# Optimization experiments

Measured on AMD Instinct MI355X. Metric: run time of the kernel, lower is better.

## Reference

```python
import jax, jax.numpy as jnp
import numpy as np

# ---- quantization constants (8-bit, per-tensor affine; representative values) ----
Q_MAX = 255.0
S_IN, Z_IN = 0.05, 128.0      # block input
S1, Z1 = 0.04, 128.0          # after expand 1x1 + hardswish
S2, Z2 = 0.04, 128.0          # after depthwise 5x5 + hardswish
S_SE1, Z_SE1 = 0.03, 128.0    # SE fc1 output
S_SE2, Z_SE2 = 1.0 / 255.0, 0.0  # SE fc2 hardsigmoid output in [0,1]
S_MUL, Z_MUL = 0.04, 128.0    # SE gated activation
S3, Z3 = 0.05, 128.0          # after project 1x1
S_OUT, Z_OUT = 0.06, 128.0    # after residual add
W_SCALE = 0.01                # symmetric per-tensor weight scale (zero_point = 0)
EXP_C = 576                   # expanded channels (depthwise groups)


def conv(x, w, stride=1, padding=0, groups=1):
    return jax.lax.conv_general_dilated(
        x, w, (stride, stride), [(padding, padding), (padding, padding)],
        feature_group_count=groups, dimension_numbers=('NCHW', 'OIHW', 'NCHW'))


def hardswish(x):
    return x * jnp.clip(x + 3.0, 0.0, 6.0) * (1.0 / 6.0)


def hardsigmoid(x):
    return jnp.clip(x + 3.0, 0.0, 6.0) * (1.0 / 6.0)


def qconv(x_q, w_q, b_q, s_in, z_in, s_out, z_out, stride=1, padding=0, groups=1, act=None):
    """Quantized conv: int-domain accumulation (simulated in fp32), fused activation
    on the dequantized accumulator, then requantize to [0, Q_MAX]."""
    acc = conv(x_q - z_in, w_q, stride, padding, groups) + b_q[None, :, None, None]
    deq = acc * (s_in * W_SCALE)  # dequantize accumulator
    if act == 'hardswish':
        deq = hardswish(deq)
    elif act == 'hardsigmoid':
        deq = hardsigmoid(deq)
    return jnp.clip(deq * (1.0 / s_out) + z_out, 0.0, Q_MAX)


def setup_inputs() -> dict:
    key = jax.random.key(0)
    ks = jax.random.split(key, 11)
    def qw(k, shape):  # int8-style symmetric weights stored as fp32 integers
        return jnp.round(jnp.clip(jax.random.normal(k, shape) * 40.0, -127.0, 127.0))
    def qb(k, n):      # int32-style bias in accumulator domain
        return jnp.round(jax.random.normal(k, (n,)) * 500.0)
    return {
        'x':      jnp.round(jax.random.uniform(ks[0], (64, 96, 28, 28)) * Q_MAX),
        'w_exp':  qw(ks[1], (576, 96, 1, 1)),  'b_exp':  qb(ks[2], 576),
        'w_dw':   qw(ks[3], (576, 1, 5, 5)),   'b_dw':   qb(ks[4], 576),
        'w_se1':  qw(ks[5], (144, 576, 1, 1)), 'b_se1':  qb(ks[6], 144),
        'w_se2':  qw(ks[7], (576, 144, 1, 1)), 'b_se2':  qb(ks[8], 576),
        'w_proj': qw(ks[9], (96, 576, 1, 1)),  'b_proj': qb(ks[10], 96),
    }


def reference(x, w_exp, b_exp, w_dw, b_dw, w_se1, b_se1, w_se2, b_se2, w_proj, b_proj):
    # expand 1x1 (+ hardswish)
    e = qconv(x, w_exp, b_exp, S_IN, Z_IN, S1, Z1, act='hardswish')
    # depthwise 5x5, padding=(5-1)//2=2, groups=expanded (+ hardswish)
    d = qconv(e, w_dw, b_dw, S1, Z1, S2, Z2, padding=2, groups=EXP_C, act='hardswish')
    # squeeze-excitation: global avg pool -> fc1 -> fc2(hardsigmoid) -> quantized mul
    pooled = jnp.mean(d, axis=(2, 3), keepdims=True)  # [N, 576, 1, 1]
    g1 = qconv(pooled, w_se1, b_se1, S2, Z2, S_SE1, Z_SE1)
    g2 = qconv(g1, w_se2, b_se2, S_SE1, Z_SE1, S_SE2, Z_SE2, act='hardsigmoid')
    gated = jnp.clip((g2 - Z_SE2) * (d - Z2) * (S_SE2 * S2 / S_MUL) + Z_MUL, 0.0, Q_MAX)
    # project 1x1 (linear)
    p = qconv(gated, w_proj, b_proj, S_MUL, Z_MUL, S3, Z3)
    # quantized residual add (stride=1, in==out channels -> use_res_connect)
    out = jnp.clip((x - Z_IN) * (S_IN / S_OUT) + (p - Z3) * (S3 / S_OUT) + Z_OUT, 0.0, Q_MAX)
    return out
```

## Files before the change

### kernel.cpp

```cpp
#include <hip/hip_runtime.h>

typedef _Float16 v8h __attribute__((ext_vector_type(8)));
typedef _Float16 v4h __attribute__((ext_vector_type(4)));
typedef _Float16 v4h_a4 __attribute__((ext_vector_type(4), aligned(4)));
typedef _Float16 v2h __attribute__((ext_vector_type(2)));
typedef float v4f __attribute__((ext_vector_type(4)));

#define NB 64
#define CI 96
#define CE 576
#define CO 96
#define HW 784
#define SEC 144

#if defined(__has_builtin)
#if __has_builtin(__builtin_amdgcn_fdot2)
#define HAVE_FDOT2 1
#endif
#endif

__device__ __forceinline__ float fdot2(v2h a, v2h b, float c) {
#ifdef HAVE_FDOT2
  return __builtin_amdgcn_fdot2(a, b, c, false);
#else
  return (float)a[0] * (float)b[0] + ((float)a[1] * (float)b[1] + c);
#endif
}

__global__ __launch_bounds__(256) void k0_cvt_w(const float* __restrict__ w_exp,
                                                const float* __restrict__ w_proj,
                                                _Float16* __restrict__ w_exp_h,
                                                _Float16* __restrict__ w_proj_h) {
  int i = blockIdx.x * 256 + threadIdx.x;
  if (i < CE * CI) {
    w_exp_h[i]  = (_Float16)w_exp[i];
    w_proj_h[i] = (_Float16)w_proj[i];
  }
}

__global__ __launch_bounds__(384) void k1_expand(const float* __restrict__ x,
                                                 const _Float16* __restrict__ w_exp_h,
                                                 const float* __restrict__ b_exp,
                                                 _Float16* __restrict__ e_s) {
  __shared__ _Float16 xf[3 * 7 * 520];
  const int tid = threadIdx.x;
  const int n   = blockIdx.z;
  const int co0 = blockIdx.y * 96;
  const int hw0 = blockIdx.x * 112;

#pragma unroll
  for (int it = 0; it < 7; ++it) {
    int idx = it * 384 + tid;
    int c = idx / 28, seg = idx % 28;
    const float4 v = *(const float4*)&x[(n * CI + c) * HW + hw0 + seg * 4];
    int s = c >> 5, q = (c >> 3) & 3, j = c & 7;
    int t = seg >> 2, l0 = (seg & 3) * 4;
    int base = (s * 7 + t) * 520 + (q * 16 + l0) * 8 + j;
    xf[base]      = (_Float16)(v.x - 128.0f);
    xf[base + 8]  = (_Float16)(v.y - 128.0f);
    xf[base + 16] = (_Float16)(v.z - 128.0f);
    xf[base + 24] = (_Float16)(v.w - 128.0f);
  }
  __syncthreads();

  const int wv = tid >> 6, lane = tid & 63;
  const int l15 = lane & 15, q = lane >> 4;

  const _Float16* wrow = &w_exp_h[(co0 + wv * 16 + l15) * CI + q * 8];
  v8h a0 = *(const v8h*)(wrow);
  v8h a1 = *(const v8h*)(wrow + 32);
  v8h a2 = *(const v8h*)(wrow + 64);

  v4f acc[7];
#pragma unroll
  for (int t = 0; t < 7; ++t) acc[t] = (v4f){0.f, 0.f, 0.f, 0.f};

#pragma unroll
  for (int t = 0; t < 7; ++t) {
    v8h b0 = *(const v8h*)&xf[(0 * 7 + t) * 520 + lane * 8];
    v8h b1 = *(const v8h*)&xf[(1 * 7 + t) * 520 + lane * 8];
    v8h b2 = *(const v8h*)&xf[(2 * 7 + t) * 520 + lane * 8];
    acc[t] = __builtin_amdgcn_mfma_f32_16x16x32_f16(a0, b0, acc[t], 0, 0, 0);
    acc[t] = __builtin_amdgcn_mfma_f32_16x16x32_f16(a1, b1, acc[t], 0, 0, 0);
    acc[t] = __builtin_amdgcn_mfma_f32_16x16x32_f16(a2, b2, acc[t], 0, 0, 0);
  }

  float bia[4];
#pragma unroll
  for (int r = 0; r < 4; ++r) bia[r] = b_exp[co0 + wv * 16 + q * 4 + r];

#pragma unroll
  for (int t = 0; t < 7; ++t) {
#pragma unroll
    for (int r = 0; r < 4; ++r) {
      int co = co0 + wv * 16 + q * 4 + r;
      int hw = hw0 + t * 16 + l15;
      float deq = (acc[t][r] + bia[r]) * 5.0e-4f;
      float cl  = fminf(fmaxf(deq + 3.0f, 0.0f), 6.0f);
      float hs  = deq * cl * (1.0f / 6.0f);
      float ev  = fminf(fmaxf(hs * 25.0f, -128.0f), 127.0f);
      e_s[(n * CE + co) * HW + hw] = (_Float16)ev;
    }
  }
}

__global__ __launch_bounds__(256, 5) void k2_dw(const _Float16* __restrict__ e_s,
                                                const float* __restrict__ w_dw,
                                                const float* __restrict__ b_dw,
                                                _Float16* __restrict__ d_t,
                                                float* __restrict__ d_sums) {
  __shared__ _Float16 e_lds[8][32][36];
  __shared__ _Float16 w_pairs[8][5][8];
  __shared__ _Float16 d_tile[8][784];
  const int tid = threadIdx.x;
  const int n = blockIdx.y;
  const int c0 = blockIdx.x * 8;

  {
    unsigned long long* z = (unsigned long long*)&e_lds[0][0][0];
    for (int idx = tid; idx < 8 * 32 * 36 * 2 / 8; idx += 256) z[idx] = 0ull;
  }
  for (int idx = tid; idx < 320; idx += 256) {
    int c = idx / 40, r = idx % 40, dy = r / 8, k = r % 8;
    int tap = (k < 4) ? k : (k - 3);
    w_pairs[c][dy][k] = (_Float16)w_dw[(c0 + c) * 25 + dy * 5 + tap];
  }
  __syncthreads();
  for (int idx = tid; idx < 1568; idx += 256) {
    int c = idx / 196, r = idx % 196, y = r / 7, j = r % 7;
    v4h v = *(const v4h*)&e_s[(n * CE + c0 + c) * HW + y * 28 + j * 4];
    *(v4h_a4*)&e_lds[c][2 + y][6 + j * 4] = v;
  }
  __syncthreads();

  const int c = tid >> 5, l = tid & 31;
  v2h W01[5], W23[5], W12[5], W34[5];
  float W0s[5], W4s[5];
#pragma unroll
  for (int dy = 0; dy < 5; ++dy) {
    W01[dy] = *(const v2h*)&w_pairs[c][dy][0];
    W23[dy] = *(const v2h*)&w_pairs[c][dy][2];
    W12[dy] = *(const v2h*)&w_pairs[c][dy][4];
    W34[dy] = *(const v2h*)&w_pairs[c][dy][6];
    W0s[dy] = (float)W01[dy][0];
    W4s[dy] = (float)W34[dy][1];
  }
  const float bc = b_dw[c0 + c];

  float csum = 0.0f;
  if (l < 28) {
    const int y = l;
    v2h P0[5], P1[5], P2[5], P3[5];
#pragma unroll
    for (int dy = 0; dy < 5; ++dy) {
      const _Float16* row = &e_lds[c][y + dy][0];
      v4h w01 = *(const v4h*)(row + 4);
      v4h w23 = *(const v4h*)(row + 8);
      P0[dy] = (v2h){w01[0], w01[1]};
      P1[dy] = (v2h){w01[2], w01[3]};
      P2[dy] = (v2h){w23[0], w23[1]};
      P3[dy] = (v2h){w23[2], w23[3]};
    }
#pragma unroll
    for (int x0 = 0; x0 < 28; x0 += 4) {
      float o0 = bc, o1 = bc, o2 = bc, o3 = bc;
#pragma unroll
      for (int dy = 0; dy < 5; ++dy) {
        o0 = fdot2(P0[dy], W01[dy], o0);
        o0 = fdot2(P1[dy], W23[dy], o0);
        o0 += (float)P2[dy][0] * W4s[dy];
        o1 += (float)P0[dy][1] * W0s[dy];
        o1 = fdot2(P1[dy], W12[dy], o1);
        o1 = fdot2(P2[dy], W34[dy], o1);
        o2 = fdot2(P1[dy], W01[dy], o2);
        o2 = fdot2(P2[dy], W23[dy], o2);
        o2 += (float)P3[dy][0] * W4s[dy];
        o3 += (float)P1[dy][1] * W0s[dy];
        o3 = fdot2(P2[dy], W12[dy], o3);
        o3 = fdot2(P3[dy], W34[dy], o3);
      }
      v4h dv;
      float oo[4] = {o0, o1, o2, o3};
#pragma unroll
      for (int i = 0; i < 4; ++i) {
        float deq = oo[i] * 4.0e-4f;
        float cl  = fminf(fmaxf(deq + 3.0f, 0.0f), 6.0f);
        float dvv = fminf(fmaxf(deq * cl * (25.0f / 6.0f), -128.0f), 127.0f);
        dv[i] = (_Float16)dvv;
        csum += dvv;
      }
      *(v4h*)&d_tile[c][y * 28 + x0] = dv;
      if (x0 < 24) {
#pragma unroll
        for (int dy = 0; dy < 5; ++dy) {
          const _Float16* row = &e_lds[c][y + dy][0];
          v4h nw = *(const v4h*)(row + x0 + 12);
          P0[dy] = P2[dy];
          P1[dy] = P3[dy];
          P2[dy] = (v2h){nw[0], nw[1]};
          P3[dy] = (v2h){nw[2], nw[3]};
        }
      }
    }
  }
#pragma unroll
  for (int m = 16; m >= 1; m >>= 1) csum += __shfl_xor(csum, m);
  if (l == 0) d_sums[n * CE + c0 + c] = csum;

  __syncthreads();
  const size_t obase = ((size_t)n * 72 + (c0 >> 3)) * 784;
  for (int hw = tid; hw < 784; hw += 256) {
    v8h o;
#pragma unroll
    for (int j = 0; j < 8; ++j) o[j] = d_tile[j][hw];
    *(v8h*)&d_t[(obase + hw) * 8] = o;
  }
}

__global__ __launch_bounds__(256) void k3a_fc1(const float* __restrict__ d_sums,
                                               const float* __restrict__ w_se1,
                                               const float* __restrict__ b_se1,
                                               float* __restrict__ g1) {
  const int tid = threadIdx.x;
  const int wv = tid >> 6, lane = tid & 63;
  const int n = blockIdx.y;
  const int o = blockIdx.x * 4 + wv;
  const float* wrow = &w_se1[o * CE];
  const float* srow = &d_sums[n * CE];
  float p = 0.f;
#pragma unroll
  for (int s = 0; s < 9; ++s) {
    int cc = lane + s * 64;
    p += wrow[cc] * srow[cc];
  }
#pragma unroll
  for (int m = 32; m >= 1; m >>= 1) p += __shfl_xor(p, m);
  if (lane == 0) {
    float deq = (p * (1.0f / 784.0f) + b_se1[o]) * 4.0e-4f;
    g1[n * SEC + o] = fminf(fmaxf(deq * 33.3333333f + 128.0f, 0.0f), 255.0f) - 128.0f;
  }
}

__global__ __launch_bounds__(256) void k3b_fc2(const float* __restrict__ g1,
                                               const float* __restrict__ w_se2,
                                               const float* __restrict__ b_se2,
                                               _Float16* __restrict__ g2h) {
  const int tid = threadIdx.x;
  const int wv = tid >> 6, lane = tid & 63;
  const int n = blockIdx.y;
  const int o = blockIdx.x * 4 + wv;
  const float* wrow = &w_se2[o * SEC];
  const float* grow = &g1[n * SEC];
  float p = wrow[lane] * grow[lane] + wrow[lane + 64] * grow[lane + 64];
  if (lane < 16) p += wrow[lane + 128] * grow[lane + 128];
#pragma unroll
  for (int m = 32; m >= 1; m >>= 1) p += __shfl_xor(p, m);
  if (lane == 0) {
    float deq = (p + b_se2[o]) * 3.0e-4f;
    g2h[n * CE + o] =
        (_Float16)(fminf(fmaxf(deq + 3.0f, 0.0f), 6.0f) * (1.0f / 6.0f));
  }
}

__global__ __launch_bounds__(192) void k4_proj(const _Float16* __restrict__ d_t,
                                               const _Float16* __restrict__ g2h,
                                               const _Float16* __restrict__ w_proj_h,
                                               const float* __restrict__ b_proj,
                                               const float* __restrict__ x,
                                               float* __restrict__ out) {
  const int tid = threadIdx.x;
  const int n = blockIdx.z;
  const int co0 = blockIdx.y * 48;
  const int hw0 = blockIdx.x * 112;
  const int wv = tid >> 6, lane = tid & 63;
  const int l15 = lane & 15, q = lane >> 4;

  v4f acc[7];
#pragma unroll
  for (int t = 0; t < 7; ++t) acc[t] = (v4f){0.f, 0.f, 0.f, 0.f};

  const _Float16* dbase = d_t + (((size_t)n * 72 + q) * 784 + hw0 + l15) * 8;
  const _Float16* abase = &w_proj_h[(co0 + wv * 16 + l15) * CE + q * 8];
  const _Float16* gbase = &g2h[(size_t)n * CE + q * 8];

  for (int ks = 0; ks < 18; ++ks) {
    v8h a = *(const v8h*)(abase + ks * 32);
    v8h g = *(const v8h*)(gbase + ks * 32);
    v8h ag = a * g;
    const _Float16* dk = dbase + (size_t)ks * (4 * 784 * 8);
#pragma unroll
    for (int t = 0; t < 7; ++t) {
      v8h b = *(const v8h*)(dk + t * (16 * 8));
      acc[t] = __builtin_amdgcn_mfma_f32_16x16x32_f16(ag, b, acc[t], 0, 0, 0);
    }
  }

  float bia[4];
#pragma unroll
  for (int r = 0; r < 4; ++r) bia[r] = b_proj[co0 + wv * 16 + q * 4 + r];

#pragma unroll
  for (int t = 0; t < 7; ++t) {
#pragma unroll
    for (int r = 0; r < 4; ++r) {
      int co = co0 + wv * 16 + q * 4 + r;
      int hw = hw0 + t * 16 + l15;
      float p = fminf(fmaxf((acc[t][r] + bia[r]) * 4.0e-4f * 20.0f + 128.0f, 0.0f), 255.0f);
      float xv = x[(n * CO + co) * HW + hw];
      float o = (xv - 128.0f) * 0.8333333333f + (p - 128.0f) * 0.8333333333f + 128.0f;
      out[(n * CO + co) * HW + hw] = fminf(fmaxf(o, 0.0f), 255.0f);
    }
  }
}

extern "C" void kernel_launch(void* const* d_in, const int* in_sizes, int n_in,
                              void* d_out, int out_size, void* d_ws, size_t ws_size,
                              hipStream_t stream) {
  const float* x      = (const float*)d_in[0];
  const float* w_exp  = (const float*)d_in[1];
  const float* b_exp  = (const float*)d_in[2];
  const float* w_dw   = (const float*)d_in[3];
  const float* b_dw   = (const float*)d_in[4];
  const float* w_se1  = (const float*)d_in[5];
  const float* b_se1  = (const float*)d_in[6];
  const float* w_se2  = (const float*)d_in[7];
  const float* b_se2  = (const float*)d_in[8];
  const float* w_proj = (const float*)d_in[9];
  const float* b_proj = (const float*)d_in[10];
  float* out = (float*)d_out;

  char* ws = (char*)d_ws;
  const size_t SZ_W  = (size_t)CE * CI * 2;
  const size_t SZ_ED = (size_t)NB * CE * HW * 2;
  const size_t SZ_S  = (size_t)NB * CE * 4;
  _Float16* w_exp_h  = (_Float16*)(ws);
  _Float16* w_proj_h = (_Float16*)(ws + SZ_W);
  _Float16* e_s      = (_Float16*)(ws + 2 * SZ_W);
  _Float16* d_t      = (_Float16*)(ws + 2 * SZ_W + SZ_ED);
  float*    d_sums   = (float*)   (ws + 2 * SZ_W + 2 * SZ_ED);
  float*    g1       = (float*)   (ws + 2 * SZ_W + 2 * SZ_ED + SZ_S);
  _Float16* g2h      = (_Float16*)(ws + 2 * SZ_W + 2 * SZ_ED + 2 * SZ_S);

  k0_cvt_w<<<(CE * CI + 255) / 256, 256, 0, stream>>>(w_exp, w_proj, w_exp_h, w_proj_h);
  k1_expand<<<dim3(7, 6, NB), 384, 0, stream>>>(x, w_exp_h, b_exp, e_s);
  k2_dw<<<dim3(72, NB), 256, 0, stream>>>(e_s, w_dw, b_dw, d_t, d_sums);
  k3a_fc1<<<dim3(36, NB), 256, 0, stream>>>(d_sums, w_se1, b_se1, g1);
  k3b_fc2<<<dim3(144, NB), 256, 0, stream>>>(g1, w_se2, b_se2, g2h);
  k4_proj<<<dim3(7, 2, NB), 192, 0, stream>>>(d_t, g2h, w_proj_h, b_proj, x, out);
}
```

Measured before the change: 191.7 us.

## Fuse expand 1x1 conv into depthwise kernel via LDS, pre-pack input to fp16

Adds a small pack kernel that converts x to fp16 in the MFMA B-operand layout. The expand 1x1 MFMA and depthwise 5x5 are merged into one kernel that handles 16 channels per block and writes the hardswish-quantized expand output straight into LDS. This removes the round trip of the large e_s intermediate through global memory. In exchange, each block re-reads the packed input for its channel group, and the larger LDS footprint and 512-thread blocks may reduce occupancy.

```diff
diff --git a/kernel.cpp b/kernel.cpp
--- a/kernel.cpp
+++ b/kernel.cpp
@@ -38,98 +38,92 @@
   }
 }
 
-__global__ __launch_bounds__(384) void k1_expand(const float* __restrict__ x,
-                                                 const _Float16* __restrict__ w_exp_h,
-                                                 const float* __restrict__ b_exp,
-                                                 _Float16* __restrict__ e_s) {
-  __shared__ _Float16 xf[3 * 7 * 520];
-  const int tid = threadIdx.x;
-  const int n   = blockIdx.z;
-  const int co0 = blockIdx.y * 96;
+__global__ __launch_bounds__(256) void k0x_pack(const float* __restrict__ x,
+                                                _Float16* __restrict__ x_f) {
+  __shared__ _Float16 xl[112][104];
+  const int tid = threadIdx.x;
+  const int n = blockIdx.y;
   const int hw0 = blockIdx.x * 112;
 
-#pragma unroll
-  for (int it = 0; it < 7; ++it) {
-    int idx = it * 384 + tid;
+  for (int idx = tid; idx < CI * 28; idx += 256) {
     int c = idx / 28, seg = idx % 28;
     const float4 v = *(const float4*)&x[(n * CI + c) * HW + hw0 + seg * 4];
-    int s = c >> 5, q = (c >> 3) & 3, j = c & 7;
-    int t = seg >> 2, l0 = (seg & 3) * 4;
-    int base = (s * 7 + t) * 520 + (q * 16 + l0) * 8 + j;
-    xf[base]      = (_Float16)(v.x - 128.0f);
-    xf[base + 8]  = (_Float16)(v.y - 128.0f);
-    xf[base + 16] = (_Float16)(v.z - 128.0f);
-    xf[base + 24] = (_Float16)(v.w - 128.0f);
+    int row = seg * 4;
+    xl[row + 0][c] = (_Float16)(v.x - 128.0f);
+    xl[row + 1][c] = (_Float16)(v.y - 128.0f);
+    xl[row + 2][c] = (_Float16)(v.z - 128.0f);
+    xl[row + 3][c] = (_Float16)(v.w - 128.0f);
   }
   __syncthreads();
 
-  const int wv = tid >> 6, lane = tid & 63;
-  const int l15 = lane & 15, q = lane >> 4;
-
-  const _Float16* wrow = &w_exp_h[(co0 + wv * 16 + l15) * CI + q * 8];
-  v8h a0 = *(const v8h*)(wrow);
-  v8h a1 = *(const v8h*)(wrow + 32);
-  v8h a2 = *(const v8h*)(wrow + 64);
-
-  v4f acc[7];
-#pragma unroll
-  for (int t = 0; t < 7; ++t) acc[t] = (v4f){0.f, 0.f, 0.f, 0.f};
-
-#pragma unroll
-  for (int t = 0; t < 7; ++t) {
-    v8h b0 = *(const v8h*)&xf[(0 * 7 + t) * 520 + lane * 8];
-    v8h b1 = *(const v8h*)&xf[(1 * 7 + t) * 520 + lane * 8];
-    v8h b2 = *(const v8h*)&xf[(2 * 7 + t) * 520 + lane * 8];
-    acc[t] = __builtin_amdgcn_mfma_f32_16x16x32_f16(a0, b0, acc[t], 0, 0, 0);
-    acc[t] = __builtin_amdgcn_mfma_f32_16x16x32_f16(a1, b1, acc[t], 0, 0, 0);
-    acc[t] = __builtin_amdgcn_mfma_f32_16x16x32_f16(a2, b2, acc[t], 0, 0, 0);
-  }
-
-  float bia[4];
-#pragma unroll
-  for (int r = 0; r < 4; ++r) bia[r] = b_exp[co0 + wv * 16 + q * 4 + r];
-
-#pragma unroll
-  for (int t = 0; t < 7; ++t) {
-#pragma unroll
-    for (int r = 0; r < 4; ++r) {
-      int co = co0 + wv * 16 + q * 4 + r;
-      int hw = hw0 + t * 16 + l15;
-      float deq = (acc[t][r] + bia[r]) * 5.0e-4f;
-      float cl  = fminf(fmaxf(deq + 3.0f, 0.0f), 6.0f);
-      float hs  = deq * cl * (1.0f / 6.0f);
-      float ev  = fminf(fmaxf(hs * 25.0f, -128.0f), 127.0f);
-      e_s[(n * CE + co) * HW + hw] = (_Float16)ev;
-    }
-  }
-}
-
-__global__ __launch_bounds__(256, 5) void k2_dw(const _Float16* __restrict__ e_s,
-                                                const float* __restrict__ w_dw,
-                                                const float* __restrict__ b_dw,
-                                                _Float16* __restrict__ d_t,
-                                                float* __restrict__ d_sums) {
-  __shared__ _Float16 e_lds[8][32][36];
-  __shared__ _Float16 w_pairs[8][5][8];
-  __shared__ _Float16 d_tile[8][784];
+  for (int idx = tid; idx < 1344; idx += 256) {
+    int t_l = idx / 192, rem = idx % 192, s = rem / 64, ln = rem % 64;
+    int hw_l = t_l * 16 + (ln & 15), ci = s * 32 + (ln >> 4) * 8;
+    v8h o;
+#pragma unroll
+    for (int j = 0; j < 8; ++j) o[j] = xl[hw_l][ci + j];
+    size_t t = (size_t)(blockIdx.x * 7 + t_l);
+    *(v8h*)&x_f[(((size_t)n * 49 + t) * 3 + s) * 512 + ln * 8] = o;
+  }
+}
+
+__global__ __launch_bounds__(512, 4) void k12_fused(const _Float16* __restrict__ x_f,
+                                                    const _Float16* __restrict__ w_exp_h,
+                                                    const float* __restrict__ b_exp,
+                                                    const float* __restrict__ w_dw,
+                                                    const float* __restrict__ b_dw,
+                                                    _Float16* __restrict__ d_t,
+                                                    float* __restrict__ d_sums) {
+  __shared__ _Float16 e_lds[16][32][36];
+  __shared__ _Float16 d_tile[16][784];
+  __shared__ _Float16 w_pairs[16][5][8];
   const int tid = threadIdx.x;
   const int n = blockIdx.y;
-  const int c0 = blockIdx.x * 8;
+  const int c0 = blockIdx.x * 16;
 
   {
     unsigned long long* z = (unsigned long long*)&e_lds[0][0][0];
-    for (int idx = tid; idx < 8 * 32 * 36 * 2 / 8; idx += 256) z[idx] = 0ull;
-  }
-  for (int idx = tid; idx < 320; idx += 256) {
+    for (int idx = tid; idx < 16 * 32 * 36 * 2 / 8; idx += 512) z[idx] = 0ull;
+  }
+  for (int idx = tid; idx < 640; idx += 512) {
     int c = idx / 40, r = idx % 40, dy = r / 8, k = r % 8;
     int tap = (k < 4) ? k : (k - 3);
     w_pairs[c][dy][k] = (_Float16)w_dw[(c0 + c) * 25 + dy * 5 + tap];
   }
   __syncthreads();
-  for (int idx = tid; idx < 1568; idx += 256) {
-    int c = idx / 196, r = idx % 196, y = r / 7, j = r % 7;
-    v4h v = *(const v4h*)&e_s[(n * CE + c0 + c) * HW + y * 28 + j * 4];
-    *(v4h_a4*)&e_lds[c][2 + y][6 + j * 4] = v;
+
+  const int wv = tid >> 6, lane = tid & 63;
+  const int l15 = lane & 15, q = lane >> 4;
+
+  {
+    const _Float16* wrow = &w_exp_h[(c0 + l15) * CI + q * 8];
+    v8h a0 = *(const v8h*)(wrow);
+    v8h a1 = *(const v8h*)(wrow + 32);
+    v8h a2 = *(const v8h*)(wrow + 64);
+    float bia[4];
+#pragma unroll
+    for (int r = 0; r < 4; ++r) bia[r] = b_exp[c0 + q * 4 + r];
+
+    const _Float16* xb = x_f + (size_t)n * (49 * 3 * 512) + lane * 8;
+    for (int t = wv; t < 49; t += 8) {
+      const _Float16* xt = xb + (size_t)t * (3 * 512);
+      v8h b0 = *(const v8h*)(xt);
+      v8h b1 = *(const v8h*)(xt + 512);
+      v8h b2 = *(const v8h*)(xt + 1024);
+      v4f acc = (v4f){0.f, 0.f, 0.f, 0.f};
+      acc = __builtin_amdgcn_mfma_f32_16x16x32_f16(a0, b0, acc, 0, 0, 0);
+      acc = __builtin_amdgcn_mfma_f32_16x16x32_f16(a1, b1, acc, 0, 0, 0);
+      acc = __builtin_amdgcn_mfma_f32_16x16x32_f16(a2, b2, acc, 0, 0, 0);
+      int hw = t * 16 + l15;
+      int y = hw / 28, xx = hw - y * 28;
+#pragma unroll
+      for (int r = 0; r < 4; ++r) {
+        float deq = (acc[r] + bia[r]) * 5.0e-4f;
+        float cl  = fminf(fmaxf(deq + 3.0f, 0.0f), 6.0f);
+        float ev  = fminf(fmaxf(deq * cl * (25.0f / 6.0f), -128.0f), 127.0f);
+        e_lds[q * 4 + r][2 + y][6 + xx] = (_Float16)ev;
+      }
+    }
   }
   __syncthreads();
 
@@ -209,11 +203,12 @@
 
   __syncthreads();
   const size_t obase = ((size_t)n * 72 + (c0 >> 3)) * 784;
-  for (int hw = tid; hw < 784; hw += 256) {
-    v8h o;
-#pragma unroll
-    for (int j = 0; j < 8; ++j) o[j] = d_tile[j][hw];
-    *(v8h*)&d_t[(obase + hw) * 8] = o;
+  for (int hw = tid; hw < 784; hw += 512) {
+    v8h o0, o1;
+#pragma unroll
+    for (int j = 0; j < 8; ++j) { o0[j] = d_tile[j][hw]; o1[j] = d_tile[8 + j][hw]; }
+    *(v8h*)&d_t[(obase + hw) * 8] = o0;
+    *(v8h*)&d_t[(obase + 784 + hw) * 8] = o1;
   }
 }
 
@@ -331,19 +326,20 @@
 
   char* ws = (char*)d_ws;
   const size_t SZ_W  = (size_t)CE * CI * 2;
-  const size_t SZ_ED = (size_t)NB * CE * HW * 2;
+  const size_t SZ_XF = (size_t)NB * 49 * 3 * 512 * 2;
+  const size_t SZ_D  = (size_t)NB * CE * HW * 2;
   const size_t SZ_S  = (size_t)NB * CE * 4;
   _Float16* w_exp_h  = (_Float16*)(ws);
   _Float16* w_proj_h = (_Float16*)(ws + SZ_W);
-  _Float16* e_s      = (_Float16*)(ws + 2 * SZ_W);
-  _Float16* d_t      = (_Float16*)(ws + 2 * SZ_W + SZ_ED);
-  float*    d_sums   = (float*)   (ws + 2 * SZ_W + 2 * SZ_ED);
-  float*    g1       = (float*)   (ws + 2 * SZ_W + 2 * SZ_ED + SZ_S);
-  _Float16* g2h      = (_Float16*)(ws + 2 * SZ_W + 2 * SZ_ED + 2 * SZ_S);
+  _Float16* x_f      = (_Float16*)(ws + 2 * SZ_W);
+  _Float16* d_t      = (_Float16*)(ws + 2 * SZ_W + SZ_XF);
+  float*    d_sums   = (float*)   (ws + 2 * SZ_W + SZ_XF + SZ_D);
+  float*    g1       = (float*)   (ws + 2 * SZ_W + SZ_XF + SZ_D + SZ_S);
+  _Float16* g2h      = (_Float16*)(ws + 2 * SZ_W + SZ_XF + SZ_D + 2 * SZ_S);
 
   k0_cvt_w<<<(CE * CI + 255) / 256, 256, 0, stream>>>(w_exp, w_proj, w_exp_h, w_proj_h);
-  k1_expand<<<dim3(7, 6, NB), 384, 0, stream>>>(x, w_exp_h, b_exp, e_s);
-  k2_dw<<<dim3(72, NB), 256, 0, stream>>>(e_s, w_dw, b_dw, d_t, d_sums);
+  k0x_pack<<<dim3(7, NB), 256, 0, stream>>>(x, x_f);
+  k12_fused<<<dim3(36, NB), 512, 0, stream>>>(x_f, w_exp_h, b_exp, w_dw, b_dw, d_t, d_sums);
   k3a_fc1<<<dim3(36, NB), 256, 0, stream>>>(d_sums, w_se1, b_se1, g1);
   k3b_fc2<<<dim3(144, NB), 256, 0, stream>>>(g1, w_se2, b_se2, g2h);
   k4_proj<<<dim3(7, 2, NB), 192, 0, stream>>>(d_t, g2h, w_proj_h, b_proj, x, out);
```

Result: faster. 179.5 us (-6.4%).
